# Performance work log

Measured on AMD Instinct MI355X. Metric: run time of the kernel, lower is better.

The kernel has to match this reference:

```python
import jax, jax.numpy as jnp
import numpy as np

B, M, FIN, FOUT = 8, 2048, 256, 128
ALPHA = 0.2  # LeakyReLU negative slope
NEG_INF = -9e15


def _xavier_uniform(key, shape, gain):
    fan_in, fan_out = shape[0], shape[1]
    bound = gain * np.sqrt(6.0 / (fan_in + fan_out))
    return jax.random.uniform(key, shape, jnp.float32, -bound, bound)


def setup_inputs() -> dict:
    key = jax.random.key(0)
    k1, k2, k3, k4 = jax.random.split(key, 4)
    x = jax.random.normal(k1, (B, M, FIN), jnp.float32)
    adj1 = jax.random.randint(k2, (B, M, M), 0, 2).astype(jnp.int32)
    W = _xavier_uniform(k3, (FIN, FOUT), gain=2.0)
    a = _xavier_uniform(k4, (2 * FOUT, 1), gain=2.0)
    return {"input": x, "adj1": adj1, "W": W, "a": a}


def reference(input, adj1, W, a):
    # h: [B, M, FOUT]
    h = jnp.matmul(input, W)
    # e[b,i,j] = leakyrelu( concat(h_i, h_j) . a ) = leakyrelu( h_i.a1 + h_j.a2 )
    a1 = a[:FOUT, 0]   # [FOUT]
    a2 = a[FOUT:, 0]   # [FOUT]
    f1 = jnp.einsum('bme,e->bm', h, a1)  # source (row i) term
    f2 = jnp.einsum('bme,e->bm', h, a2)  # target (col j) term
    e = jax.nn.leaky_relu(f1[:, :, None] + f2[:, None, :], negative_slope=ALPHA)  # [B,M,M]
    scores = jnp.where(adj1 > 0, e, NEG_INF)
    attention = jax.nn.softmax(scores, axis=-1)
    # dropout is identity in eval mode (training=False)
    h_prime = jnp.matmul(attention, h)  # [B,M,FOUT]
    return jax.nn.elu(h_prime)  # concat=True branch
```

## Files before the change

### kernel.cpp

```cpp
#include <hip/hip_runtime.h>
#include <math.h>

#define B_    8
#define M_    2048
#define FIN_  256
#define FOUT_ 128
#define ALPHA_ 0.2f
#define NEG_INF_ -9.0e15f

typedef unsigned short u16;
typedef __attribute__((ext_vector_type(8))) short bf16x8;
typedef __attribute__((ext_vector_type(4))) float f32x4;

static __device__ __forceinline__ u16 f2bf(float f) {
  union { float f; unsigned u; } v; v.f = f;
  unsigned r = v.u + 0x7FFFu + ((v.u >> 16) & 1u);
  return (u16)(r >> 16);
}

__global__ __launch_bounds__(256) void k_prep(const float* __restrict__ W,
                                              u16* __restrict__ Wt) {
  const int id = blockIdx.x * 256 + threadIdx.x;
  const int f = id >> 8;
  const int k = id & 255;
  Wt[f * FIN_ + k] = f2bf(W[(size_t)k * FOUT_ + f]);
}

__global__ __launch_bounds__(256) void k_xw(const float* __restrict__ x,
                                            const u16* __restrict__ Wt,
                                            const float* __restrict__ a,
                                            u16* __restrict__ ht,
                                            float* __restrict__ f1,
                                            float* __restrict__ f2) {
  int blk = blockIdx.x;
  blk = (blk & 7) * 32 + (blk >> 3);
  const int b    = blk >> 5;
  const int row0 = blk * 64;
  const int tid  = threadIdx.x;
  const int w  = tid >> 6;
  const int l  = tid & 63;
  const int lr = l & 15;
  const int g  = l >> 4;

  f32x4 acc[8];
#pragma unroll
  for (int ft = 0; ft < 8; ++ft) acc[ft] = (f32x4){0.f, 0.f, 0.f, 0.f};

  const float* xrow = x + (size_t)(row0 + w * 16 + lr) * FIN_;
#pragma unroll
  for (int ks = 0; ks < 8; ++ks) {
    float4 xa = *(const float4*)(xrow + ks * 32 + g * 8);
    float4 xc = *(const float4*)(xrow + ks * 32 + g * 8 + 4);
    bf16x8 af;
    af[0] = (short)f2bf(xa.x); af[1] = (short)f2bf(xa.y);
    af[2] = (short)f2bf(xa.z); af[3] = (short)f2bf(xa.w);
    af[4] = (short)f2bf(xc.x); af[5] = (short)f2bf(xc.y);
    af[6] = (short)f2bf(xc.z); af[7] = (short)f2bf(xc.w);
#pragma unroll
    for (int ft = 0; ft < 8; ++ft) {
      bf16x8 bf = *(const bf16x8*)(Wt + (ft * 16 + lr) * FIN_ + ks * 32 + g * 8);
      acc[ft] = __builtin_amdgcn_mfma_f32_16x16x32_bf16(af, bf, acc[ft], 0, 0, 0);
    }
  }

  float v1[4] = {0.f, 0.f, 0.f, 0.f};
  float v2[4] = {0.f, 0.f, 0.f, 0.f};
#pragma unroll
  for (int ft = 0; ft < 8; ++ft) {
    const float a1v = a[ft * 16 + lr];
    const float a2v = a[FOUT_ + ft * 16 + lr];
#pragma unroll
    for (int j = 0; j < 4; ++j) {
      v1[j] += acc[ft][j] * a1v;
      v2[j] += acc[ft][j] * a2v;
    }
  }
#pragma unroll
  for (int off = 1; off < 16; off <<= 1) {
#pragma unroll
    for (int j = 0; j < 4; ++j) {
      v1[j] += __shfl_xor(v1[j], off);
      v2[j] += __shfl_xor(v2[j], off);
    }
  }
  if (lr == 0) {
#pragma unroll
    for (int j = 0; j < 4; ++j) {
      const int rowg = row0 + w * 16 + g * 4 + j;
      f1[rowg] = v1[j];
      f2[rowg] = v2[j];
    }
  }

  __shared__ float hs[64][130];
#pragma unroll
  for (int ft = 0; ft < 8; ++ft)
#pragma unroll
    for (int j = 0; j < 4; ++j)
      hs[w * 16 + g * 4 + j][ft * 16 + lr] = acc[ft][j];
  __syncthreads();

  const int f    = tid >> 1;
  const int half = tid & 1;
  union { u16 u[32]; uint4 q[4]; } hb;
#pragma unroll
  for (int i = 0; i < 32; ++i) hb.u[i] = f2bf(hs[half * 32 + i][f]);
  u16* dst = ht + ((size_t)(b * FOUT_ + f)) * M_ + (row0 & (M_ - 1)) + half * 32;
#pragma unroll
  for (int q = 0; q < 4; ++q) *(uint4*)(dst + q * 8) = hb.q[q];
}

__global__ __launch_bounds__(128) void k_attn(const u16* __restrict__ ht,
                                              const int* __restrict__ adj,
                                              const float* __restrict__ f1,
                                              const float* __restrict__ f2,
                                              float* __restrict__ out) {
  int blk = blockIdx.x;
  blk = (blk & 7) * 128 + (blk >> 3);
  const int b       = blk >> 7;
  const int row0loc = (blk & 127) * 16;
  const int tid = threadIdx.x;
  const int w  = tid >> 6;
  const int l  = tid & 63;
  const int lr = l & 15;
  const int g  = l >> 4;
  const int r  = tid >> 3;
  const int ts = tid & 7;

  __shared__ __align__(16) u16 P[16][128];
  __shared__ float smx[16], ssum[16], sscale[16], f1s[16];

  if (tid < 16) {
    smx[tid]  = -INFINITY;
    ssum[tid] = 0.f;
    f1s[tid]  = f1[b * M_ + row0loc + tid];
  }

  f32x4 acc[4];
#pragma unroll
  for (int ft = 0; ft < 4; ++ft) acc[ft] = (f32x4){0.f, 0.f, 0.f, 0.f};

  const int fbase = w * 64;
  const size_t adjrow = ((size_t)b * M_ + row0loc + r) * M_;
  const float* f2b = f2 + b * M_;
  char* Pb = (char*)P;

  __syncthreads();

  for (int n0 = 0; n0 < M_; n0 += 128) {
    const int c0 = n0 + ts * 8;
    const int c1 = n0 + 64 + ts * 8;
    int4 aj0 = *(const int4*)(adj + adjrow + c0);
    int4 aj1 = *(const int4*)(adj + adjrow + c0 + 4);
    int4 aj2 = *(const int4*)(adj + adjrow + c1);
    int4 aj3 = *(const int4*)(adj + adjrow + c1 + 4);
    float4 fa = *(const float4*)(f2b + c0);
    float4 fb = *(const float4*)(f2b + c0 + 4);
    float4 fc = *(const float4*)(f2b + c1);
    float4 fd = *(const float4*)(f2b + c1 + 4);
    const float f1r = f1s[r];
    int   aj[16] = {aj0.x, aj0.y, aj0.z, aj0.w, aj1.x, aj1.y, aj1.z, aj1.w,
                    aj2.x, aj2.y, aj2.z, aj2.w, aj3.x, aj3.y, aj3.z, aj3.w};
    float fv[16] = {fa.x, fa.y, fa.z, fa.w, fb.x, fb.y, fb.z, fb.w,
                    fc.x, fc.y, fc.z, fc.w, fd.x, fd.y, fd.z, fd.w};
    float s[16];
#pragma unroll
    for (int i = 0; i < 16; ++i) {
      float z = f1r + fv[i];
      float e = z > 0.f ? z : ALPHA_ * z;
      s[i] = aj[i] > 0 ? e : NEG_INF_;
    }
    float cmax = s[0];
#pragma unroll
    for (int i = 1; i < 16; ++i) cmax = fmaxf(cmax, s[i]);
#pragma unroll
    for (int off = 1; off < 8; off <<= 1) cmax = fmaxf(cmax, __shfl_xor(cmax, off));
    const float m_old = smx[r];
    const float m_new = fmaxf(m_old, cmax);
    const float scl   = __expf(m_old - m_new);
    float psum = 0.f;
#pragma unroll
    for (int i = 0; i < 16; ++i) {
      float p = __expf(s[i] - m_new);
      s[i] = p;
      psum += p;
    }
#pragma unroll
    for (int off = 1; off < 8; off <<= 1) psum += __shfl_xor(psum, off);
    if (ts == 0) {
      smx[r]    = m_new;
      ssum[r]   = ssum[r] * scl + psum;
      sscale[r] = scl;
    }
    union { u16 u[8]; uint4 q; } w0, w1;
#pragma unroll
    for (int i = 0; i < 8; ++i) { w0.u[i] = f2bf(s[i]); w1.u[i] = f2bf(s[i + 8]); }
    *(uint4*)(Pb + r * 256 + ((ts ^ (r & 7)) << 4))       = w0.q;
    *(uint4*)(Pb + r * 256 + (((ts + 8) ^ (r & 7)) << 4)) = w1.q;
    __syncthreads();

    f32x4 scv = { sscale[g * 4], sscale[g * 4 + 1], sscale[g * 4 + 2], sscale[g * 4 + 3] };
#pragma unroll
    for (int ft = 0; ft < 4; ++ft) acc[ft] *= scv;
#pragma unroll
    for (int ks = 0; ks < 4; ++ks) {
      bf16x8 af = *(const bf16x8*)(Pb + lr * 256 + (((ks * 4 + g) ^ (lr & 7)) << 4));
#pragma unroll
      for (int ft = 0; ft < 4; ++ft) {
        const u16* hp = ht + ((size_t)(b * FOUT_ + fbase + ft * 16 + lr)) * M_
                        + n0 + ks * 32 + g * 8;
        bf16x8 bv = *(const bf16x8*)hp;
        acc[ft] = __builtin_amdgcn_mfma_f32_16x16x32_bf16(af, bv, acc[ft], 0, 0, 0);
      }
    }
    __syncthreads();
  }

  f32x4 inv = { 1.f / ssum[g * 4], 1.f / ssum[g * 4 + 1],
                1.f / ssum[g * 4 + 2], 1.f / ssum[g * 4 + 3] };
#pragma unroll
  for (int ft = 0; ft < 4; ++ft) {
#pragma unroll
    for (int j = 0; j < 4; ++j) {
      float t = acc[ft][j] * inv[j];
      float o = t > 0.f ? t : __expf(t) - 1.f;
      out[((size_t)b * M_ + row0loc + g * 4 + j) * FOUT_ + fbase + ft * 16 + lr] = o;
    }
  }
}

extern "C" void kernel_launch(void* const* d_in, const int* in_sizes, int n_in,
                              void* d_out, int out_size, void* d_ws, size_t ws_size,
                              hipStream_t stream) {
  const float* x   = (const float*)d_in[0];
  const int*   adj = (const int*)d_in[1];
  const float* W   = (const float*)d_in[2];
  const float* a   = (const float*)d_in[3];
  float* out = (float*)d_out;

  char* ws = (char*)d_ws;
  u16*   Wt = (u16*)ws;
  float* f1 = (float*)(ws + 65536);
  float* f2 = (float*)(ws + 131072);
  u16*   ht = (u16*)(ws + 196608);

  hipLaunchKernelGGL(k_prep, dim3(128),  dim3(256), 0, stream, W, Wt);
  hipLaunchKernelGGL(k_xw,   dim3(256),  dim3(256), 0, stream, x, Wt, a, ht, f1, f2);
  hipLaunchKernelGGL(k_attn, dim3(1024), dim3(128), 0, stream, ht, adj, f1, f2, out);
}
```

Baseline: 256.1 us.

## Pre-convert x to bf16, shrink xw tiles, widen attention blocks with adj prefetch

Adds a conversion kernel that writes x as bf16 next to the transposed W, so k_xw loads bf16 directly. k_xw now uses 16-row tiles split over two waves, with a shared-memory reduction for f1/f2, giving four times as many blocks. k_attn moves to 256 threads, with each wave handling 32 output features, and prefetches the next adjacency and f2 chunk into registers to hide load latency. The trade-offs are an extra 8 MB bf16 round trip for x and more blocks that each re-read Wt.

Measured after the change: 263.4 us. 2.9% more time.

```diff
diff --git a/kernel.cpp b/kernel.cpp
--- a/kernel.cpp
+++ b/kernel.cpp
@@ -18,57 +18,67 @@
   return (u16)(r >> 16);
 }
 
-__global__ __launch_bounds__(256) void k_prep(const float* __restrict__ W,
+__global__ __launch_bounds__(256) void k_conv(const float* __restrict__ x,
+                                              const float* __restrict__ W,
+                                              u16* __restrict__ xbf,
                                               u16* __restrict__ Wt) {
-  const int id = blockIdx.x * 256 + threadIdx.x;
-  const int f = id >> 8;
-  const int k = id & 255;
-  Wt[f * FIN_ + k] = f2bf(W[(size_t)k * FOUT_ + f]);
-}
-
-__global__ __launch_bounds__(256) void k_xw(const float* __restrict__ x,
+  const int blk = blockIdx.x;
+  if (blk < 2048) {
+    const size_t base = ((size_t)blk * 256 + threadIdx.x) * 8;
+    float4 v0 = *(const float4*)(x + base);
+    float4 v1 = *(const float4*)(x + base + 4);
+    union { u16 u[8]; uint4 q; } o;
+    o.u[0] = f2bf(v0.x); o.u[1] = f2bf(v0.y); o.u[2] = f2bf(v0.z); o.u[3] = f2bf(v0.w);
+    o.u[4] = f2bf(v1.x); o.u[5] = f2bf(v1.y); o.u[6] = f2bf(v1.z); o.u[7] = f2bf(v1.w);
+    *(uint4*)(xbf + base) = o.q;
+  } else {
+    const int id = (blk - 2048) * 256 + threadIdx.x;
+    const int f = id >> 8;
+    const int k = id & 255;
+    Wt[f * FIN_ + k] = f2bf(W[(size_t)k * FOUT_ + f]);
+  }
+}
+
+__global__ __launch_bounds__(128) void k_xw(const u16* __restrict__ xbf,
                                             const u16* __restrict__ Wt,
                                             const float* __restrict__ a,
                                             u16* __restrict__ ht,
                                             float* __restrict__ f1,
                                             float* __restrict__ f2) {
   int blk = blockIdx.x;
-  blk = (blk & 7) * 32 + (blk >> 3);
-  const int b    = blk >> 5;
-  const int row0 = blk * 64;
+  blk = (blk & 7) * 128 + (blk >> 3);
+  const int b    = blk >> 7;
+  const int row0 = (blk & 127) * 16;
+  const int rowg = b * M_ + row0;
   const int tid  = threadIdx.x;
   const int w  = tid >> 6;
   const int l  = tid & 63;
   const int lr = l & 15;
   const int g  = l >> 4;
-
-  f32x4 acc[8];
-#pragma unroll
-  for (int ft = 0; ft < 8; ++ft) acc[ft] = (f32x4){0.f, 0.f, 0.f, 0.f};
-
-  const float* xrow = x + (size_t)(row0 + w * 16 + lr) * FIN_;
+  const int fbase = w * 64;
+
+  f32x4 acc[4];
+#pragma unroll
+  for (int ft = 0; ft < 4; ++ft) acc[ft] = (f32x4){0.f, 0.f, 0.f, 0.f};
+
+  const u16* xr = xbf + (size_t)(rowg + lr) * FIN_;
 #pragma unroll
   for (int ks = 0; ks < 8; ++ks) {
-    float4 xa = *(const float4*)(xrow + ks * 32 + g * 8);
-    float4 xc = *(const float4*)(xrow + ks * 32 + g * 8 + 4);
-    bf16x8 af;
-    af[0] = (short)f2bf(xa.x); af[1] = (short)f2bf(xa.y);
-    af[2] = (short)f2bf(xa.z); af[3] = (short)f2bf(xa.w);
-    af[4] = (short)f2bf(xc.x); af[5] = (short)f2bf(xc.y);
-    af[6] = (short)f2bf(xc.z); af[7] = (short)f2bf(xc.w);
-#pragma unroll
-    for (int ft = 0; ft < 8; ++ft) {
-      bf16x8 bf = *(const bf16x8*)(Wt + (ft * 16 + lr) * FIN_ + ks * 32 + g * 8);
+    bf16x8 af = *(const bf16x8*)(xr + ks * 32 + g * 8);
+#pragma unroll
+    for (int ft = 0; ft < 4; ++ft) {
+      bf16x8 bf = *(const bf16x8*)(Wt + (fbase + ft * 16 + lr) * FIN_ + ks * 32 + g * 8);
       acc[ft] = __builtin_amdgcn_mfma_f32_16x16x32_bf16(af, bf, acc[ft], 0, 0, 0);
     }
   }
 
+  __shared__ float sf1[2][16], sf2[2][16];
   float v1[4] = {0.f, 0.f, 0.f, 0.f};
   float v2[4] = {0.f, 0.f, 0.f, 0.f};
 #pragma unroll
-  for (int ft = 0; ft < 8; ++ft) {
-    const float a1v = a[ft * 16 + lr];
-    const float a2v = a[FOUT_ + ft * 16 + lr];
+  for (int ft = 0; ft < 4; ++ft) {
+    const float a1v = a[fbase + ft * 16 + lr];
+    const float a2v = a[FOUT_ + fbase + ft * 16 + lr];
 #pragma unroll
     for (int j = 0; j < 4; ++j) {
       v1[j] += acc[ft][j] * a1v;
@@ -86,46 +96,48 @@
   if (lr == 0) {
 #pragma unroll
     for (int j = 0; j < 4; ++j) {
-      const int rowg = row0 + w * 16 + g * 4 + j;
-      f1[rowg] = v1[j];
-      f2[rowg] = v2[j];
-    }
-  }
-
-  __shared__ float hs[64][130];
-#pragma unroll
-  for (int ft = 0; ft < 8; ++ft)
+      sf1[w][g * 4 + j] = v1[j];
+      sf2[w][g * 4 + j] = v2[j];
+    }
+  }
+
+  __shared__ float hs[16][132];
+#pragma unroll
+  for (int ft = 0; ft < 4; ++ft)
 #pragma unroll
     for (int j = 0; j < 4; ++j)
-      hs[w * 16 + g * 4 + j][ft * 16 + lr] = acc[ft][j];
+      hs[g * 4 + j][fbase + ft * 16 + lr] = acc[ft][j];
   __syncthreads();
 
-  const int f    = tid >> 1;
-  const int half = tid & 1;
-  union { u16 u[32]; uint4 q[4]; } hb;
-#pragma unroll
-  for (int i = 0; i < 32; ++i) hb.u[i] = f2bf(hs[half * 32 + i][f]);
-  u16* dst = ht + ((size_t)(b * FOUT_ + f)) * M_ + (row0 & (M_ - 1)) + half * 32;
-#pragma unroll
-  for (int q = 0; q < 4; ++q) *(uint4*)(dst + q * 8) = hb.q[q];
-}
-
-__global__ __launch_bounds__(128) void k_attn(const u16* __restrict__ ht,
+  if (tid < 16) {
+    f1[rowg + tid] = sf1[0][tid] + sf1[1][tid];
+    f2[rowg + tid] = sf2[0][tid] + sf2[1][tid];
+  }
+  const int f = tid;
+  union { u16 u[16]; uint4 q[2]; } hb;
+#pragma unroll
+  for (int i = 0; i < 16; ++i) hb.u[i] = f2bf(hs[i][f]);
+  u16* dst = ht + (size_t)(b * FOUT_ + f) * M_ + row0;
+  *(uint4*)(dst)     = hb.q[0];
+  *(uint4*)(dst + 8) = hb.q[1];
+}
+
+__global__ __launch_bounds__(256) void k_attn(const u16* __restrict__ ht,
                                               const int* __restrict__ adj,
                                               const float* __restrict__ f1,
                                               const float* __restrict__ f2,
                                               float* __restrict__ out) {
   int blk = blockIdx.x;
   blk = (blk & 7) * 128 + (blk >> 3);
-  const int b       = blk >> 7;
-  const int row0loc = (blk & 127) * 16;
+  const int b    = blk >> 7;
+  const int row0 = (blk & 127) * 16;
   const int tid = threadIdx.x;
   const int w  = tid >> 6;
   const int l  = tid & 63;
   const int lr = l & 15;
   const int g  = l >> 4;
-  const int r  = tid >> 3;
-  const int ts = tid & 7;
+  const int r  = tid >> 4;
+  const int ts = tid & 15;
 
   __shared__ __align__(16) u16 P[16][128];
   __shared__ float smx[16], ssum[16], sscale[16], f1s[16];
@@ -133,85 +145,81 @@
   if (tid < 16) {
     smx[tid]  = -INFINITY;
     ssum[tid] = 0.f;
-    f1s[tid]  = f1[b * M_ + row0loc + tid];
-  }
-
-  f32x4 acc[4];
-#pragma unroll
-  for (int ft = 0; ft < 4; ++ft) acc[ft] = (f32x4){0.f, 0.f, 0.f, 0.f};
-
-  const int fbase = w * 64;
-  const size_t adjrow = ((size_t)b * M_ + row0loc + r) * M_;
-  const float* f2b = f2 + b * M_;
+    f1s[tid]  = f1[b * M_ + row0 + tid];
+  }
+
+  f32x4 acc0 = (f32x4){0.f, 0.f, 0.f, 0.f};
+  f32x4 acc1 = (f32x4){0.f, 0.f, 0.f, 0.f};
+
+  const int fbase = w * 32;
+  const int* ap   = adj + ((size_t)b * M_ + row0 + r) * M_ + ts * 8;
+  const float* fp = f2 + b * M_ + ts * 8;
+  const u16* hp0  = ht + (size_t)(b * FOUT_ + fbase + lr) * M_ + g * 8;
+  const u16* hp1  = hp0 + 16 * M_;
   char* Pb = (char*)P;
 
+  int4   ajA = *(const int4*)(ap);
+  int4   ajB = *(const int4*)(ap + 4);
+  float4 fvA = *(const float4*)(fp);
+  float4 fvB = *(const float4*)(fp + 4);
+
   __syncthreads();
 
   for (int n0 = 0; n0 < M_; n0 += 128) {
-    const int c0 = n0 + ts * 8;
-    const int c1 = n0 + 64 + ts * 8;
-    int4 aj0 = *(const int4*)(adj + adjrow + c0);
-    int4 aj1 = *(const int4*)(adj + adjrow + c0 + 4);
-    int4 aj2 = *(const int4*)(adj + adjrow + c1);
-    int4 aj3 = *(const int4*)(adj + adjrow + c1 + 4);
-    float4 fa = *(const float4*)(f2b + c0);
-    float4 fb = *(const float4*)(f2b + c0 + 4);
-    float4 fc = *(const float4*)(f2b + c1);
-    float4 fd = *(const float4*)(f2b + c1 + 4);
+    const int   aj[8] = {ajA.x, ajA.y, ajA.z, ajA.w, ajB.x, ajB.y, ajB.z, ajB.w};
+    const float fv[8] = {fvA.x, fvA.y, fvA.z, fvA.w, fvB.x, fvB.y, fvB.z, fvB.w};
+    if (n0 + 128 < M_) {
+      ajA = *(const int4*)(ap + n0 + 128);
+      ajB = *(const int4*)(ap + n0 + 132);
+      fvA = *(const float4*)(fp + n0 + 128);
+      fvB = *(const float4*)(fp + n0 + 132);
+    }
     const float f1r = f1s[r];
-    int   aj[16] = {aj0.x, aj0.y, aj0.z, aj0.w, aj1.x, aj1.y, aj1.z, aj1.w,
-                    aj2.x, aj2.y, aj2.z, aj2.w, aj3.x, aj3.y, aj3.z, aj3.w};
-    float fv[16] = {fa.x, fa.y, fa.z, fa.w, fb.x, fb.y, fb.z, fb.w,
-                    fc.x, fc.y, fc.z, fc.w, fd.x, fd.y, fd.z, fd.w};
-    float s[16];
-#pragma unroll
-    for (int i = 0; i < 16; ++i) {
+    float s[8];
+#pragma unroll
+    for (int i = 0; i < 8; ++i) {
       float z = f1r + fv[i];
       float e = z > 0.f ? z : ALPHA_ * z;
       s[i] = aj[i] > 0 ? e : NEG_INF_;
     }
     float cmax = s[0];
 #pragma unroll
-    for (int i = 1; i < 16; ++i) cmax = fmaxf(cmax, s[i]);
-#pragma unroll
-    for (int off = 1; off < 8; off <<= 1) cmax = fmaxf(cmax, __shfl_xor(cmax, off));
+    for (int i = 1; i < 8; ++i) cmax = fmaxf(cmax, s[i]);
+#pragma unroll
+    for (int off = 1; off < 16; off <<= 1) cmax = fmaxf(cmax, __shfl_xor(cmax, off));
     const float m_old = smx[r];
     const float m_new = fmaxf(m_old, cmax);
     const float scl   = __expf(m_old - m_new);
     float psum = 0.f;
 #pragma unroll
-    for (int i = 0; i < 16; ++i) {
+    for (int i = 0; i < 8; ++i) {
       float p = __expf(s[i] - m_new);
       s[i] = p;
       psum += p;
     }
 #pragma unroll
-    for (int off = 1; off < 8; off <<= 1) psum += __shfl_xor(psum, off);
+    for (int off = 1; off < 16; off <<= 1) psum += __shfl_xor(psum, off);
     if (ts == 0) {
       smx[r]    = m_new;
       ssum[r]   = ssum[r] * scl + psum;
       sscale[r] = scl;
     }
-    union { u16 u[8]; uint4 q; } w0, w1;
-#pragma unroll
-    for (int i = 0; i < 8; ++i) { w0.u[i] = f2bf(s[i]); w1.u[i] = f2bf(s[i + 8]); }
-    *(uint4*)(Pb + r * 256 + ((ts ^ (r & 7)) << 4))       = w0.q;
-    *(uint4*)(Pb + r * 256 + (((ts + 8) ^ (r & 7)) << 4)) = w1.q;
+    union { u16 u[8]; uint4 q; } pw;
+#pragma unroll
+    for (int i = 0; i < 8; ++i) pw.u[i] = f2bf(s[i]);
+    *(uint4*)(Pb + r * 256 + ((ts ^ (r & 7)) << 4)) = pw.q;
     __syncthreads();
 
     f32x4 scv = { sscale[g * 4], sscale[g * 4 + 1], sscale[g * 4 + 2], sscale[g * 4 + 3] };
-#pragma unroll
-    for (int ft = 0; ft < 4; ++ft) acc[ft] *= scv;
+    acc0 *= scv;
+    acc1 *= scv;
 #pragma unroll
     for (int ks = 0; ks < 4; ++ks) {
       bf16x8 af = *(const bf16x8*)(Pb + lr * 256 + (((ks * 4 + g) ^ (lr & 7)) << 4));
-#pragma unroll
-      for (int ft = 0; ft < 4; ++ft) {
-        const u16* hp = ht + ((size_t)(b * FOUT_ + fbase + ft * 16 + lr)) * M_
-                        + n0 + ks * 32 + g * 8;
-        bf16x8 bv = *(const bf16x8*)hp;
-        acc[ft] = __builtin_amdgcn_mfma_f32_16x16x32_bf16(af, bv, acc[ft], 0, 0, 0);
-      }
+      bf16x8 b0 = *(const bf16x8*)(hp0 + n0 + ks * 32);
+      bf16x8 b1 = *(const bf16x8*)(hp1 + n0 + ks * 32);
+      acc0 = __builtin_amdgcn_mfma_f32_16x16x32_bf16(af, b0, acc0, 0, 0, 0);
+      acc1 = __builtin_amdgcn_mfma_f32_16x16x32_bf16(af, b1, acc1, 0, 0, 0);
     }
     __syncthreads();
   }
@@ -219,13 +227,12 @@
   f32x4 inv = { 1.f / ssum[g * 4], 1.f / ssum[g * 4 + 1],
                 1.f / ssum[g * 4 + 2], 1.f / ssum[g * 4 + 3] };
 #pragma unroll
-  for (int ft = 0; ft < 4; ++ft) {
-#pragma unroll
-    for (int j = 0; j < 4; ++j) {
-      float t = acc[ft][j] * inv[j];
-      float o = t > 0.f ? t : __expf(t) - 1.f;
-      out[((size_t)b * M_ + row0loc + g * 4 + j) * FOUT_ + fbase + ft * 16 + lr] = o;
-    }
+  for (int j = 0; j < 4; ++j) {
+    const size_t orow = ((size_t)b * M_ + row0 + g * 4 + j) * FOUT_;
+    float t0 = acc0[j] * inv[j];
+    float t1 = acc1[j] * inv[j];
+    out[orow + fbase + lr]      = t0 > 0.f ? t0 : __expf(t0) - 1.f;
+    out[orow + fbase + 16 + lr] = t1 > 0.f ? t1 : __expf(t1) - 1.f;
   }
 }
 
@@ -239,12 +246,13 @@
   float* out = (float*)d_out;
 
   char* ws = (char*)d_ws;
-  u16*   Wt = (u16*)ws;
-  float* f1 = (float*)(ws + 65536);
-  float* f2 = (float*)(ws + 131072);
-  u16*   ht = (u16*)(ws + 196608);
-
-  hipLaunchKernelGGL(k_prep, dim3(128),  dim3(256), 0, stream, W, Wt);
-  hipLaunchKernelGGL(k_xw,   dim3(256),  dim3(256), 0, stream, x, Wt, a, ht, f1, f2);
-  hipLaunchKernelGGL(k_attn, dim3(1024), dim3(128), 0, stream, ht, adj, f1, f2, out);
-}
+  u16*   Wt  = (u16*)ws;
+  float* f1  = (float*)(ws + 65536);
+  float* f2  = (float*)(ws + 131072);
+  u16*   ht  = (u16*)(ws + 196608);
+  u16*   xbf = (u16*)(ws + 196608 + 8388608);
+
+  hipLaunchKernelGGL(k_conv, dim3(2176), dim3(256), 0, stream, x, W, xbf, Wt);
+  hipLaunchKernelGGL(k_xw,   dim3(1024), dim3(128), 0, stream, xbf, Wt, a, ht, f1, f2);
+  hipLaunchKernelGGL(k_attn, dim3(1024), dim3(256), 0, stream, ht, adj, f1, f2, out);
+}
```
